# Kernel optimization log

Hardware: AMD Instinct MI355X
Metric: run time of the kernel (lower is better)

Reference implementation:

```python
import jax, jax.numpy as jnp
import numpy as np

NUM_HEADS = 8
KEY_DIM = 16
D = 32          # attn_ratio * key_dim
DH = D * NUM_HEADS  # 256
NH_KD = KEY_DIM * NUM_HEADS  # 128
DIM = 256


def _conv1x1_bn(x, W, s, b):
    # 1x1 conv (no bias) followed by eval-mode BatchNorm folded to affine.
    # x: [B, Cin, H, W], W: [Cout, Cin], s/b: [Cout]
    y = jnp.einsum('oc,bchw->bohw', W, x)
    return y * s[None, :, None, None] + b[None, :, None, None]


def setup_inputs() -> dict:
    key = jax.random.key(0)
    ks = jax.random.split(key, 16)
    B, C, H, Wd = 2, DIM, 64, 64
    rgb = jax.random.normal(ks[0], (B, C, H, Wd), dtype=jnp.float32)
    edge = jax.random.normal(ks[1], (B, C, H, Wd), dtype=jnp.float32)

    def conv_w(k, o, i):
        return jax.random.normal(k, (o, i), dtype=jnp.float32) * (1.0 / np.sqrt(i))

    def bn(k, c):
        k1, k2 = jax.random.split(k)
        s = jax.random.uniform(k1, (c,), dtype=jnp.float32, minval=0.5, maxval=1.5)
        b = jax.random.normal(k2, (c,), dtype=jnp.float32) * 0.1
        return s, b

    Wq = conv_w(ks[2], NH_KD, C); sq, bq = bn(ks[3], NH_KD)
    Wk = conv_w(ks[4], NH_KD, C); sk, bk = bn(ks[5], NH_KD)
    Wv = conv_w(ks[6], DH, C);   sv, bv = bn(ks[7], DH)
    Wp = conv_w(ks[8], C, DH);   sp, bp = bn(ks[9], C)
    return dict(rgb=rgb, edge=edge, Wq=Wq, sq=sq, bq=bq, Wk=Wk, sk=sk, bk=bk,
                Wv=Wv, sv=sv, bv=bv, Wp=Wp, sp=sp, bp=bp)


def reference(rgb, edge, Wq, sq, bq, Wk, sk, bk, Wv, sv, bv, Wp, sp, bp):
    B, C, H, Wd = rgb.shape
    N = H * Wd
    # Q from rgb, K/V from edge (all 1x1 conv + BN)
    qq = _conv1x1_bn(rgb, Wq, sq, bq).reshape(B, NUM_HEADS, KEY_DIM, N)
    qq = jnp.transpose(qq, (0, 1, 3, 2))                       # [B,h,N,kd]
    kk = _conv1x1_bn(edge, Wk, sk, bk).reshape(B, NUM_HEADS, KEY_DIM, N)  # [B,h,kd,N]
    vv = _conv1x1_bn(edge, Wv, sv, bv).reshape(B, NUM_HEADS, D, N)
    vv = jnp.transpose(vv, (0, 1, 3, 2))                       # [B,h,N,d]
    # NOTE: original forward does NOT apply self.scale -- faithful omission.
    attn = jnp.einsum('bhnk,bhkm->bhnm', qq, kk)               # [B,h,N,N]
    attn = jax.nn.softmax(attn, axis=-1)
    xx = jnp.einsum('bhnm,bhmd->bhnd', attn, vv)               # [B,h,N,d]
    xx = jnp.transpose(xx, (0, 1, 3, 2)).reshape(B, DH, H, Wd)
    xx = jax.nn.relu(xx)                                       # activation before proj conv
    xx = _conv1x1_bn(xx, Wp, sp, bp)                           # [B,C,H,W]
    return xx
```

## Files before the change

kernel.cpp:

```cpp
#include <hip/hip_runtime.h>
#include <hip/hip_bf16.h>

#define NB 2
#define CIN 256
#define NPIX 4096
#define NHEADS 8
#define KD 16
#define DV 32
#define DH 256
#define NHKD 128

typedef short bf16x8 __attribute__((ext_vector_type(8)));
typedef short s16x4 __attribute__((ext_vector_type(4)));
typedef float f32x2 __attribute__((ext_vector_type(2)));
typedef float f32x4 __attribute__((ext_vector_type(4)));
typedef float f32x16 __attribute__((ext_vector_type(16)));
typedef unsigned int u32x2 __attribute__((ext_vector_type(2)));
typedef unsigned int u32x4 __attribute__((ext_vector_type(4)));

#define LOG2E 1.4426950408889634f

static __device__ __forceinline__ unsigned short f2bf(float f) {
    __hip_bfloat16 h = __float2bfloat16(f);
    return __builtin_bit_cast(unsigned short, h);
}

static __device__ __forceinline__ unsigned pack_rhu(float lo, float hi) {
    unsigned a = __builtin_bit_cast(unsigned, lo) + 0x8000u;
    unsigned b = __builtin_bit_cast(unsigned, hi) + 0x8000u;
    return (a >> 16) | (b & 0xffff0000u);
}

__global__ __launch_bounds__(256) void k_prep(
    const float* __restrict__ Wq, const float* __restrict__ Wk,
    const float* __restrict__ Wv, const float* __restrict__ Wp,
    unsigned short* __restrict__ wq, unsigned short* __restrict__ wk,
    unsigned short* __restrict__ wv, unsigned short* __restrict__ wp)
{
    int i = blockIdx.x * 256 + threadIdx.x;
    if (i < NHKD * CIN) { wq[i] = f2bf(Wq[i]); wk[i] = f2bf(Wk[i]); }
    if (i < DH * CIN)   { wv[i] = f2bf(Wv[i]); wp[i] = f2bf(Wp[i]); }
}

__global__ __launch_bounds__(256) void k_qkv(
    const float* __restrict__ rgb, const float* __restrict__ edge,
    const unsigned short* __restrict__ wq, const unsigned short* __restrict__ wk,
    const unsigned short* __restrict__ wv,
    const float* __restrict__ sq, const float* __restrict__ bq,
    const float* __restrict__ sk, const float* __restrict__ bk,
    const float* __restrict__ sv, const float* __restrict__ bv,
    unsigned short* __restrict__ Qw, unsigned short* __restrict__ Kw,
    unsigned short* __restrict__ Vw)
{
    const int nb = blockIdx.x;
    const int ob = blockIdx.y;
    const int b  = blockIdx.z;
    const int tid = threadIdx.x;
    const int wave = tid >> 6, lane = tid & 63;
    const int cl = lane & 15, g = lane >> 4;

    const float* X; const unsigned short* W; const float* sc; const float* bi;
    int obase, job;
    if (ob < 2)      { X = rgb  + (size_t)b*CIN*NPIX; W = wq; sc = sq; bi = bq; obase = ob*64;     job = 0; }
    else if (ob < 4) { X = edge + (size_t)b*CIN*NPIX; W = wk; sc = sk; bi = bk; obase = (ob-2)*64; job = 1; }
    else             { X = edge + (size_t)b*CIN*NPIX; W = wv; sc = sv; bi = bv; obase = (ob-4)*64; job = 2; }

    __shared__ float xt[32 * 65];

    f32x4 acc[4];
    #pragma unroll
    for (int i = 0; i < 4; i++) acc[i] = (f32x4)0.f;

    const int n0 = nb * 64;
    const int ow = obase + wave * 16 + cl;
    const unsigned short* Wrow = W + (size_t)ow * CIN;

    for (int kt = 0; kt < 8; kt++) {
        __syncthreads();
        {
            int tr = tid >> 6;
            int tc = tid & 63;
            #pragma unroll
            for (int r = 0; r < 8; r++) {
                int c_local = r * 4 + tr;
                xt[c_local * 65 + tc] = X[(size_t)(kt * 32 + c_local) * NPIX + n0 + tc];
            }
        }
        __syncthreads();
        #pragma unroll
        for (int ns = 0; ns < 4; ns++) {
            u32x4 aw;
            #pragma unroll
            for (int w = 0; w < 4; w++)
                aw[w] = pack_rhu(xt[(8 * g + 2 * w) * 65 + ns * 16 + cl],
                                 xt[(8 * g + 2 * w + 1) * 65 + ns * 16 + cl]);
            bf16x8 a = __builtin_bit_cast(bf16x8, aw);
            bf16x8 wfrag = *reinterpret_cast<const bf16x8*>(Wrow + kt * 32 + 8 * g);
            acc[ns] = __builtin_amdgcn_mfma_f32_16x16x32_bf16(a, wfrag, acc[ns], 0, 0, 0);
        }
    }

    const float sco = sc[ow], bio = bi[ow];
    if (job == 2) {
        int h = ow >> 5, d = ow & 31;
        unsigned short* dst = Vw + ((size_t)((b * 8 + h) * 32 + d)) * NPIX;
        #pragma unroll
        for (int ns = 0; ns < 4; ns++) {
            int nr = n0 + ns * 16 + 4 * g;
            s16x4 pk;
            #pragma unroll
            for (int r = 0; r < 4; r++) pk[r] = (short)f2bf(acc[ns][r] * sco + bio);
            *reinterpret_cast<s16x4*>(dst + nr) = pk;
        }
    } else {
        float scq = sco, biq = bio;
        if (job == 0) { scq *= LOG2E; biq *= LOG2E; }
        unsigned short* base = (job == 0) ? Qw : Kw;
        int h = ow >> 4, kd = ow & 15;
        unsigned short* dst = base + ((size_t)(b * 8 + h) * NPIX) * KD + kd;
        #pragma unroll
        for (int ns = 0; ns < 4; ns++)
            #pragma unroll
            for (int r = 0; r < 4; r++) {
                int nr = n0 + ns * 16 + 4 * g + r;
                dst[(size_t)nr * KD] = f2bf(acc[ns][r] * scq + biq);
            }
    }
}

typedef const unsigned int __attribute__((address_space(1)))* gp_t;
typedef unsigned int __attribute__((address_space(3)))* lp_t;

__global__ __launch_bounds__(256) void k_attn(
    const unsigned short* __restrict__ Qw, const unsigned short* __restrict__ Kw,
    const unsigned short* __restrict__ Vw, unsigned short* __restrict__ Ow)
{
    const int qg = blockIdx.x;
    const int bh = blockIdx.y;
    const int tid = threadIdx.x;
    const int wave = tid >> 6, lane = tid & 63;
    const int l31 = lane & 31, hi = lane >> 5;

    __shared__ union {
        unsigned short v[4][2][2048];
        struct { float o[4][32][32]; float l[4][32]; } c;
    } sh;

    const unsigned short* Kbase = Kw + (size_t)bh * NPIX * KD;
    const unsigned short* Vbase = Vw + (size_t)bh * DV * NPIX;

    const int q0 = qg * 32;
    const bf16x8 qf = *(const bf16x8*)(Qw + ((size_t)bh * NPIX + q0 + l31) * KD + 8 * hi);

    const unsigned short* Kln = Kbase + (size_t)l31 * KD + 8 * hi;
#define KF0(T) (*(const bf16x8*)(Kln + ((T) * 64 + 0) * KD))
#define KF1(T) (*(const bf16x8*)(Kln + ((T) * 64 + 32) * KD))

    const int scb = ((lane & 7) * 16) ^ ((lane >> 3) << 4);
    const unsigned short* Vln = Vbase + (size_t)(lane >> 3) * NPIX + (scb >> 1);
#define STAGE(T, BUF) do { _Pragma("unroll") for (int j = 0; j < 4; ++j) \
    __builtin_amdgcn_global_load_lds( \
        (gp_t)(const void*)(Vln + (size_t)j * 8 * NPIX + (size_t)(T) * 64), \
        (lp_t)(void*)(&sh.v[wave][BUF][j * 512]), 16, 0, 0); } while (0)

    const int vsw = (l31 & 7) << 4;

    f32x16 o = (f32x16)0.f;
    float l_run = 0.f;
    const f32x16 z16 = (f32x16)0.f;

    const int T0 = wave * 16;
    bf16x8 ka0 = KF0(T0), ka1 = KF1(T0);
    bf16x8 kb0, kb1;
    STAGE(T0, 0);

    #pragma unroll
    for (int t = 0; t < 16; ++t) {
        const int T = T0 + t;
        const int cur = t & 1;
        if (t < 15) {
            kb0 = KF0(T + 1);
            kb1 = KF1(T + 1);
            STAGE(T + 1, cur ^ 1);
        }

        __builtin_amdgcn_s_setprio(1);
        f32x16 s0 = __builtin_amdgcn_mfma_f32_32x32x16_bf16(ka0, qf, z16, 0, 0, 0);
        f32x16 s1 = __builtin_amdgcn_mfma_f32_32x32x16_bf16(ka1, qf, z16, 0, 0, 0);
        __builtin_amdgcn_s_setprio(0);
        #pragma unroll
        for (int i = 0; i < 16; ++i) s0[i] = __builtin_amdgcn_exp2f(s0[i]);
        #pragma unroll
        for (int i = 0; i < 16; ++i) s1[i] = __builtin_amdgcn_exp2f(s1[i]);

        f32x2 r[8];
        #pragma unroll
        for (int i = 0; i < 8; ++i) {
            f32x2 a = {s0[2*i], s0[2*i+1]};
            f32x2 b = {s1[2*i], s1[2*i+1]};
            r[i] = a + b;
        }
        r[0] += r[4]; r[1] += r[5]; r[2] += r[6]; r[3] += r[7];
        r[0] += r[2]; r[1] += r[3];
        r[0] += r[1];
        l_run += r[0].x + r[0].y;

        unsigned up[16];
        #pragma unroll
        for (int ss = 0; ss < 8; ++ss) {
            up[ss]     = pack_rhu(s0[2*ss], s0[2*ss+1]);
            up[8 + ss] = pack_rhu(s1[2*ss], s1[2*ss+1]);
        }
        #pragma unroll
        for (int gg = 0; gg < 4; ++gg) {
            u32x2 r0 = __builtin_amdgcn_permlane32_swap(up[4*gg+0], up[4*gg+2], false, false);
            up[4*gg+0] = r0.x; up[4*gg+2] = r0.y;
            u32x2 r1 = __builtin_amdgcn_permlane32_swap(up[4*gg+1], up[4*gg+3], false, false);
            up[4*gg+1] = r1.x; up[4*gg+3] = r1.y;
        }

        asm volatile("s_waitcnt vmcnt(0)" ::: "memory");

        __builtin_amdgcn_s_setprio(1);
        #pragma unroll
        for (int c = 0; c < 4; ++c) {
            u32x4 av;
            av.x = up[4*c + 0];
            av.y = up[4*c + 1];
            av.z = up[4*c + 2];
            av.w = up[4*c + 3];
            const int vidx = (l31 * 128 + ((32 * c + 16 * hi) ^ vsw)) >> 1;
            bf16x8 vb = *(const bf16x8*)(&sh.v[wave][cur][vidx]);
            o = __builtin_amdgcn_mfma_f32_32x32x16_bf16(
                    __builtin_bit_cast(bf16x8, av), vb, o, 0, 0, 0);
        }
        __builtin_amdgcn_s_setprio(0);
        ka0 = kb0; ka1 = kb1;
    }
#undef KF0
#undef KF1
#undef STAGE

    l_run += __shfl_xor(l_run, 32, 64);

    __syncthreads();
    #pragma unroll
    for (int r = 0; r < 16; ++r) {
        const int qr = (r & 3) + 8 * (r >> 2) + 4 * hi;
        sh.c.o[wave][qr][l31] = o[r];
    }
    if (hi == 0) sh.c.l[wave][l31] = l_run;
    __syncthreads();

    const int q = tid >> 3;
    const int d0 = (tid & 7) * 4;
    const float lsum = sh.c.l[0][q] + sh.c.l[1][q] + sh.c.l[2][q] + sh.c.l[3][q];
    const float linv = __builtin_amdgcn_rcpf(lsum);
    float v[4];
    #pragma unroll
    for (int i = 0; i < 4; ++i) {
        float s = sh.c.o[0][q][d0+i] + sh.c.o[1][q][d0+i] + sh.c.o[2][q][d0+i] + sh.c.o[3][q][d0+i];
        v[i] = fmaxf(s * linv, 0.f);
    }
    const int b = bh >> 3, h = bh & 7;
    u32x2 pk;
    pk.x = (unsigned)f2bf(v[0]) | ((unsigned)f2bf(v[1]) << 16);
    pk.y = (unsigned)f2bf(v[2]) | ((unsigned)f2bf(v[3]) << 16);
    *reinterpret_cast<u32x2*>(Ow + ((size_t)b * NPIX + q0 + q) * DH + h * DV + d0) = pk;
}

__global__ __launch_bounds__(256) void k_proj(
    const unsigned short* __restrict__ Xo, const unsigned short* __restrict__ wp,
    const float* __restrict__ sp, const float* __restrict__ bp,
    float* __restrict__ out)
{
    const int nb = blockIdx.x;
    const int b  = blockIdx.y;
    const int tid = threadIdx.x;
    const int wave = tid >> 6, lane = tid & 63;
    const int cl = lane & 15, g = lane >> 4;

    const int cbase = wave * 64;
    f32x4 acc[4][2];
    #pragma unroll
    for (int i = 0; i < 4; i++)
        #pragma unroll
        for (int j = 0; j < 2; j++) acc[i][j] = (f32x4)0.f;

    const unsigned short* Xb = Xo + ((size_t)b * NPIX + nb * 32) * DH;

    #pragma unroll
    for (int kt = 0; kt < 8; kt++) {
        bf16x8 afr[4];
        #pragma unroll
        for (int cs = 0; cs < 4; cs++)
            afr[cs] = *reinterpret_cast<const bf16x8*>(wp + (size_t)(cbase + cs * 16 + cl) * DH + kt * 32 + 8 * g);
        #pragma unroll
        for (int ns = 0; ns < 2; ns++) {
            bf16x8 bfr = *reinterpret_cast<const bf16x8*>(Xb + (size_t)(ns * 16 + cl) * DH + kt * 32 + 8 * g);
            #pragma unroll
            for (int cs = 0; cs < 4; cs++)
                acc[cs][ns] = __builtin_amdgcn_mfma_f32_16x16x32_bf16(afr[cs], bfr, acc[cs][ns], 0, 0, 0);
        }
    }

    #pragma unroll
    for (int cs = 0; cs < 4; cs++)
        #pragma unroll
        for (int r = 0; r < 4; r++) {
            int c = cbase + cs * 16 + 4 * g + r;
            float scv = sp[c], biv = bp[c];
            float* dst = out + ((size_t)b * DH + c) * NPIX + nb * 32;
            #pragma unroll
            for (int ns = 0; ns < 2; ns++)
                dst[ns * 16 + cl] = acc[cs][ns][r] * scv + biv;
        }
}

extern "C" void kernel_launch(void* const* d_in, const int* in_sizes, int n_in,
                              void* d_out, int out_size, void* d_ws, size_t ws_size,
                              hipStream_t stream) {
    const float* rgb  = (const float*)d_in[0];
    const float* edge = (const float*)d_in[1];
    const float* Wq = (const float*)d_in[2];
    const float* sq = (const float*)d_in[3];
    const float* bq = (const float*)d_in[4];
    const float* Wk = (const float*)d_in[5];
    const float* sk = (const float*)d_in[6];
    const float* bk = (const float*)d_in[7];
    const float* Wv = (const float*)d_in[8];
    const float* sv = (const float*)d_in[9];
    const float* bv = (const float*)d_in[10];
    const float* Wp = (const float*)d_in[11];
    const float* sp = (const float*)d_in[12];
    const float* bp = (const float*)d_in[13];
    float* out = (float*)d_out;

    char* ws = (char*)d_ws;
    unsigned short* wq = (unsigned short*)(ws + 0);
    unsigned short* wk = (unsigned short*)(ws + (64 << 10));
    unsigned short* wv = (unsigned short*)(ws + (128 << 10));
    unsigned short* wp = (unsigned short*)(ws + (256 << 10));
    size_t o = 384 << 10;
    unsigned short* Qw = (unsigned short*)(ws + o); o += (size_t)16 * NPIX * KD * 2;
    unsigned short* Kw = (unsigned short*)(ws + o); o += (size_t)16 * NPIX * KD * 2;
    unsigned short* Vw = (unsigned short*)(ws + o); o += (size_t)16 * DV * NPIX * 2;
    unsigned short* Ow = (unsigned short*)(ws + o);

    k_prep<<<dim3(256), dim3(256), 0, stream>>>(Wq, Wk, Wv, Wp, wq, wk, wv, wp);
    k_qkv<<<dim3(64, 8, NB), dim3(256), 0, stream>>>(rgb, edge, wq, wk, wv,
                                                     sq, bq, sk, bk, sv, bv, Qw, Kw, Vw);
    k_attn<<<dim3(128, 16), dim3(256), 0, stream>>>(Qw, Kw, Vw, Ow);
    k_proj<<<dim3(128, NB), dim3(256), 0, stream>>>(Ow, wp, sp, bp, out);
}
```

Before: 91.67 us.

## Interleave QK and PV MFMA halves in attention loop and raise occupancy

Splits each 64-key tile of the attention loop into two 32-key halves. The exp/pack/permute work on the first half now overlaps with the second QK MFMA, and its PV MFMAs are issued before the second half's softmax. K fragments are loaded from global memory at the start of each iteration instead of being prefetched a tile ahead, and launch bounds request 4 blocks per SM. The aim is to cut register pressure and hide transcendental latency behind matrix work, at the cost of exposing K load latency inside each iteration.

```diff
diff --git a/kernel.cpp b/kernel.cpp
--- a/kernel.cpp
+++ b/kernel.cpp
@@ -131,7 +131,7 @@
 typedef const unsigned int __attribute__((address_space(1)))* gp_t;
 typedef unsigned int __attribute__((address_space(3)))* lp_t;
 
-__global__ __launch_bounds__(256) void k_attn(
+__global__ __launch_bounds__(256, 4) void k_attn(
     const unsigned short* __restrict__ Qw, const unsigned short* __restrict__ Kw,
     const unsigned short* __restrict__ Vw, unsigned short* __restrict__ Ow)
 {
@@ -170,72 +170,99 @@
     const f32x16 z16 = (f32x16)0.f;
 
     const int T0 = wave * 16;
-    bf16x8 ka0 = KF0(T0), ka1 = KF1(T0);
-    bf16x8 kb0, kb1;
     STAGE(T0, 0);
 
     #pragma unroll
     for (int t = 0; t < 16; ++t) {
         const int T = T0 + t;
         const int cur = t & 1;
-        if (t < 15) {
-            kb0 = KF0(T + 1);
-            kb1 = KF1(T + 1);
-            STAGE(T + 1, cur ^ 1);
-        }
+        bf16x8 ka0 = KF0(T);
+        bf16x8 ka1 = KF1(T);
+        if (t < 15) STAGE(T + 1, cur ^ 1);
 
         __builtin_amdgcn_s_setprio(1);
         f32x16 s0 = __builtin_amdgcn_mfma_f32_32x32x16_bf16(ka0, qf, z16, 0, 0, 0);
+        __builtin_amdgcn_s_setprio(0);
+        #pragma unroll
+        for (int i = 0; i < 16; ++i) s0[i] = __builtin_amdgcn_exp2f(s0[i]);
+        {
+            f32x2 p[4];
+            #pragma unroll
+            for (int j = 0; j < 4; ++j) {
+                f32x2 a = {s0[2*j], s0[2*j+1]};
+                f32x2 b = {s0[2*j+8], s0[2*j+9]};
+                p[j] = a + b;
+            }
+            p[0] += p[2]; p[1] += p[3]; p[0] += p[1];
+            l_run += p[0].x + p[0].y;
+        }
+        unsigned u0[8];
+        #pragma unroll
+        for (int ss = 0; ss < 8; ++ss) u0[ss] = pack_rhu(s0[2*ss], s0[2*ss+1]);
+        #pragma unroll
+        for (int gg = 0; gg < 2; ++gg) {
+            u32x2 r0 = __builtin_amdgcn_permlane32_swap(u0[4*gg+0], u0[4*gg+2], false, false);
+            u0[4*gg+0] = r0.x; u0[4*gg+2] = r0.y;
+            u32x2 r1 = __builtin_amdgcn_permlane32_swap(u0[4*gg+1], u0[4*gg+3], false, false);
+            u0[4*gg+1] = r1.x; u0[4*gg+3] = r1.y;
+        }
+
+        __builtin_amdgcn_s_setprio(1);
         f32x16 s1 = __builtin_amdgcn_mfma_f32_32x32x16_bf16(ka1, qf, z16, 0, 0, 0);
         __builtin_amdgcn_s_setprio(0);
-        #pragma unroll
-        for (int i = 0; i < 16; ++i) s0[i] = __builtin_amdgcn_exp2f(s0[i]);
+        asm volatile("s_waitcnt vmcnt(0)" ::: "memory");
+
+        __builtin_amdgcn_s_setprio(1);
+        {
+            u32x4 av;
+            av.x = u0[0]; av.y = u0[1]; av.z = u0[2]; av.w = u0[3];
+            const int vi0 = (l31 * 128 + ((16 * hi) ^ vsw)) >> 1;
+            bf16x8 vb0 = *(const bf16x8*)(&sh.v[wave][cur][vi0]);
+            o = __builtin_amdgcn_mfma_f32_32x32x16_bf16(__builtin_bit_cast(bf16x8, av), vb0, o, 0, 0, 0);
+            av.x = u0[4]; av.y = u0[5]; av.z = u0[6]; av.w = u0[7];
+            const int vi1 = (l31 * 128 + ((32 + 16 * hi) ^ vsw)) >> 1;
+            bf16x8 vb1 = *(const bf16x8*)(&sh.v[wave][cur][vi1]);
+            o = __builtin_amdgcn_mfma_f32_32x32x16_bf16(__builtin_bit_cast(bf16x8, av), vb1, o, 0, 0, 0);
+        }
+        __builtin_amdgcn_s_setprio(0);
+
         #pragma unroll
         for (int i = 0; i < 16; ++i) s1[i] = __builtin_amdgcn_exp2f(s1[i]);
-
-        f32x2 r[8];
-        #pragma unroll
-        for (int i = 0; i < 8; ++i) {
-            f32x2 a = {s0[2*i], s0[2*i+1]};
-            f32x2 b = {s1[2*i], s1[2*i+1]};
-            r[i] = a + b;
-        }
-        r[0] += r[4]; r[1] += r[5]; r[2] += r[6]; r[3] += r[7];
-        r[0] += r[2]; r[1] += r[3];
-        r[0] += r[1];
-        l_run += r[0].x + r[0].y;
-
-        unsigned up[16];
-        #pragma unroll
-        for (int ss = 0; ss < 8; ++ss) {
-            up[ss]     = pack_rhu(s0[2*ss], s0[2*ss+1]);
-            up[8 + ss] = pack_rhu(s1[2*ss], s1[2*ss+1]);
-        }
-        #pragma unroll
-        for (int gg = 0; gg < 4; ++gg) {
-            u32x2 r0 = __builtin_amdgcn_permlane32_swap(up[4*gg+0], up[4*gg+2], false, false);
-            up[4*gg+0] = r0.x; up[4*gg+2] = r0.y;
-            u32x2 r1 = __builtin_amdgcn_permlane32_swap(up[4*gg+1], up[4*gg+3], false, false);
-            up[4*gg+1] = r1.x; up[4*gg+3] = r1.y;
-        }
-
-        asm volatile("s_waitcnt vmcnt(0)" ::: "memory");
+        {
+            f32x2 p[4];
+            #pragma unroll
+            for (int j = 0; j < 4; ++j) {
+                f32x2 a = {s1[2*j], s1[2*j+1]};
+                f32x2 b = {s1[2*j+8], s1[2*j+9]};
+                p[j] = a + b;
+            }
+            p[0] += p[2]; p[1] += p[3]; p[0] += p[1];
+            l_run += p[0].x + p[0].y;
+        }
+        unsigned u1[8];
+        #pragma unroll
+        for (int ss = 0; ss < 8; ++ss) u1[ss] = pack_rhu(s1[2*ss], s1[2*ss+1]);
+        #pragma unroll
+        for (int gg = 0; gg < 2; ++gg) {
+            u32x2 r0 = __builtin_amdgcn_permlane32_swap(u1[4*gg+0], u1[4*gg+2], false, false);
+            u1[4*gg+0] = r0.x; u1[4*gg+2] = r0.y;
+            u32x2 r1 = __builtin_amdgcn_permlane32_swap(u1[4*gg+1], u1[4*gg+3], false, false);
+            u1[4*gg+1] = r1.x; u1[4*gg+3] = r1.y;
+        }
 
         __builtin_amdgcn_s_setprio(1);
-        #pragma unroll
-        for (int c = 0; c < 4; ++c) {
+        {
             u32x4 av;
-            av.x = up[4*c + 0];
-            av.y = up[4*c + 1];
-            av.z = up[4*c + 2];
-            av.w = up[4*c + 3];
-            const int vidx = (l31 * 128 + ((32 * c + 16 * hi) ^ vsw)) >> 1;
-            bf16x8 vb = *(const bf16x8*)(&sh.v[wave][cur][vidx]);
-            o = __builtin_amdgcn_mfma_f32_32x32x16_bf16(
-                    __builtin_bit_cast(bf16x8, av), vb, o, 0, 0, 0);
+            av.x = u1[0]; av.y = u1[1]; av.z = u1[2]; av.w = u1[3];
+            const int vi2 = (l31 * 128 + ((64 + 16 * hi) ^ vsw)) >> 1;
+            bf16x8 vb2 = *(const bf16x8*)(&sh.v[wave][cur][vi2]);
+            o = __builtin_amdgcn_mfma_f32_32x32x16_bf16(__builtin_bit_cast(bf16x8, av), vb2, o, 0, 0, 0);
+            av.x = u1[4]; av.y = u1[5]; av.z = u1[6]; av.w = u1[7];
+            const int vi3 = (l31 * 128 + ((96 + 16 * hi) ^ vsw)) >> 1;
+            bf16x8 vb3 = *(const bf16x8*)(&sh.v[wave][cur][vi3]);
+            o = __builtin_amdgcn_mfma_f32_32x32x16_bf16(__builtin_bit_cast(bf16x8, av), vb3, o, 0, 0, 0);
         }
         __builtin_amdgcn_s_setprio(0);
-        ka0 = kb0; ka1 = kb1;
     }
 #undef KF0
 #undef KF1
```

After: 88.80 us. 3.1% less time.
